# Performance work log

Hardware: AMD Instinct MI355X
Metric: run time of the kernel (lower is better)

Reference implementation:

```python
import jax, jax.numpy as jnp
import numpy as np


def setup_inputs() -> dict:
    key = jax.random.key(0)
    k1, k2, k3 = jax.random.split(key, 3)
    B, S_enc, S_dec, D = 8, 4096, 4096, 128
    b = jax.random.normal(k1, (B, S_enc, D), dtype=jnp.float32)
    h = jax.random.normal(k2, (B, S_dec, D), dtype=jnp.float32)
    W_b = jax.random.normal(k3, (D, D), dtype=jnp.float32) * (1.0 / np.sqrt(D))
    return {"b": b, "h": h, "W_b": W_b}


def reference(b, h, W_b):
    # tmp1 = h @ W_b : [B, S_dec, D]
    tmp1 = jnp.einsum('btd,de->bte', h, W_b)
    # scores = tmp1 @ b^T : [B, S_dec, S_enc]
    scores = jnp.einsum('bte,bse->bts', tmp1, b)
    attn = jax.nn.softmax(scores, axis=-1)
    # weighted sum over encoder positions (the original does this via a huge
    # tile/broadcast/multiply/reduce_sum; math is a batched matmul)
    cxt = jnp.einsum('bts,bsd->btd', attn, b)
    return cxt
```

## Files before the change

kernel.cpp:

```cpp
#include <hip/hip_runtime.h>

typedef _Float16 half2v __attribute__((ext_vector_type(2)));
typedef _Float16 half4 __attribute__((ext_vector_type(4)));
typedef _Float16 half8 __attribute__((ext_vector_type(8)));
typedef float floatx4 __attribute__((ext_vector_type(4)));

#define B_   8
#define SE   4096
#define SD   4096
#define D_   128
#define NT   64
#define LDB  136
#define LOG2E 1.44269504f

__device__ __forceinline__ void cp16_async(const _Float16* g, _Float16* l) {
    __builtin_amdgcn_global_load_lds((const __attribute__((address_space(1))) unsigned int*)g,
                                     (__attribute__((address_space(3))) unsigned int*)l, 16, 0, 0);
}

__global__ __launch_bounds__(256) void wprep(const float* __restrict__ W,
                                             _Float16* __restrict__ W16,
                                             _Float16* __restrict__ Wlo) {
    int i = blockIdx.x * 256 + threadIdx.x;
    float w = W[i];
    _Float16 hi = (_Float16)w;
    W16[i] = hi;
    Wlo[i] = (_Float16)(w - (float)hi);
}

__global__ __launch_bounds__(256) void kvprep(const float* __restrict__ b,
                                              const _Float16* __restrict__ W16,
                                              const _Float16* __restrict__ Wlo,
                                              _Float16* __restrict__ kp,
                                              _Float16* __restrict__ vT) {
    __shared__ _Float16 bs[64 * LDB];
    const int bb = blockIdx.y, s0 = blockIdx.x * 64;
    const int tid = threadIdx.x, wave = tid >> 6, lane = tid & 63;
    const int l15 = lane & 15, quad = lane >> 4;

    const float* bg = b + ((size_t)bb * SE + s0) * D_;
    #pragma unroll
    for (int it = 0; it < 4; ++it) {
        int idx = tid + it * 256;
        int row = idx >> 4, seg = idx & 15;
        const float* src = bg + row * D_ + seg * 8;
        float4 a = *(const float4*)src;
        float4 c = *(const float4*)(src + 4);
        half8 hv;
        hv[0] = (_Float16)a.x; hv[1] = (_Float16)a.y; hv[2] = (_Float16)a.z; hv[3] = (_Float16)a.w;
        hv[4] = (_Float16)c.x; hv[5] = (_Float16)c.y; hv[6] = (_Float16)c.z; hv[7] = (_Float16)c.w;
        *(half8*)(bs + row * LDB + seg * 8) = hv;
    }
    __syncthreads();

    half8 af[4];
    #pragma unroll
    for (int ks = 0; ks < 4; ++ks)
        af[ks] = *(const half8*)(bs + (wave * 16 + l15) * LDB + ks * 32 + quad * 8);
    floatx4 acc[8];
    #pragma unroll
    for (int nt = 0; nt < 8; ++nt) acc[nt] = (floatx4){0.f, 0.f, 0.f, 0.f};
    #pragma unroll
    for (int ks = 0; ks < 4; ++ks) {
        #pragma unroll
        for (int nt = 0; nt < 8; ++nt) {
            half8 bh = *(const half8*)(W16 + (size_t)(nt * 16 + l15) * 128 + ks * 32 + quad * 8);
            half8 bl = *(const half8*)(Wlo + (size_t)(nt * 16 + l15) * 128 + ks * 32 + quad * 8);
            acc[nt] = __builtin_amdgcn_mfma_f32_16x16x32_f16(af[ks], bh, acc[nt], 0, 0, 0);
            acc[nt] = __builtin_amdgcn_mfma_f32_16x16x32_f16(af[ks], bl, acc[nt], 0, 0, 0);
        }
    }

    {
        const int sq = tid & 15, dg = tid >> 4;
        half8 rowv[4];
        #pragma unroll
        for (int j = 0; j < 4; ++j)
            rowv[j] = *(const half8*)(bs + (sq * 4 + j) * LDB + dg * 8);
        #pragma unroll
        for (int r = 0; r < 8; ++r) {
            int d = dg * 8 + r;
            half4 o;
            #pragma unroll
            for (int j = 0; j < 4; ++j) o[j] = rowv[j][r];
            *(half4*)(vT + ((size_t)bb * D_ + d) * SE + s0 + sq * 4) = o;
        }
    }
    __syncthreads();

    #pragma unroll
    for (int nt = 0; nt < 8; ++nt)
        #pragma unroll
        for (int r = 0; r < 4; ++r)
            bs[(wave * 16 + quad * 4 + r) * LDB + nt * 16 + l15] = (_Float16)acc[nt][r];
    __syncthreads();
    _Float16* kg = kp + ((size_t)bb * SE + s0) * D_;
    {
        const int row = tid >> 2;
        #pragma unroll
        for (int it = 0; it < 4; ++it) {
            int ch = (tid & 3) + it * 4;
            half8 v = *(const half8*)(bs + row * LDB + ch * 8);
            *(half8*)(kg + row * D_ + ch * 8) = v;
        }
    }
}

__global__ __launch_bounds__(512, 4) void flash(const float* __restrict__ h,
                                                const _Float16* __restrict__ k,
                                                const _Float16* __restrict__ vT,
                                                float* __restrict__ out) {
    __shared__ _Float16 KV[2][16384];

    const int bb   = blockIdx.y;
    const int q0   = blockIdx.x * 64;
    const int tid  = threadIdx.x;
    const int wave = tid >> 6;
    const int wq   = wave >> 1;
    const int ws   = wave & 1;
    const int lane = tid & 63;
    const int l15  = lane & 15;
    const int quad = lane >> 4;

    const _Float16* kbase = k + (size_t)bb * SE * D_;
    const _Float16* vbase = vT + (size_t)bb * D_ * SE;

    int koff[2], voff[2];
    #pragma unroll
    for (int it = 0; it < 2; ++it) {
        int i = it * 512 + wave * 64 + lane;
        int kr = i >> 4, kpp = i & 15;
        koff[it] = kr * D_ + (kpp ^ (kr & 15)) * 8;
        int vr = i >> 3, vpp = i & 7;
        voff[it] = vr * SE + (vpp ^ (vr & 7)) * 8;
    }

    const _Float16* kA0[4]; const _Float16* kA1[4];
    const _Float16* vB0[2]; const _Float16* vB1[2];
    #pragma unroll
    for (int ks = 0; ks < 4; ++ks) {
        int o = l15 * 128 + (((ks * 4 + quad) ^ l15) * 8) + ws * 4096;
        kA0[ks] = &KV[0][o]; kA1[ks] = &KV[1][o];
    }
    #pragma unroll
    for (int stl = 0; stl < 2; ++stl) {
        int o = 8192 + l15 * 64 + (((ws * 4 + stl * 2 + (quad >> 1)) ^ (l15 & 7)) * 8) + (quad & 1) * 4;
        vB0[stl] = &KV[0][o]; vB1[stl] = &KV[1][o];
    }

    {
        _Float16* buf0 = &KV[0][0];
        #pragma unroll
        for (int it = 0; it < 2; ++it) {
            cp16_async(kbase + koff[it], buf0 + (it * 512 + wave * 64) * 8);
            cp16_async(vbase + voff[it], buf0 + 8192 + (it * 512 + wave * 64) * 8);
        }
    }

    half8 qf[4];
    {
        const float* hrow = h + ((size_t)bb * SD + q0 + wq * 16 + l15) * D_;
        #pragma unroll
        for (int ks = 0; ks < 4; ++ks) {
            float4 a = *(const float4*)(hrow + ks * 32 + quad * 8);
            float4 c = *(const float4*)(hrow + ks * 32 + quad * 8 + 4);
            half8 f;
            f[0] = (_Float16)(a.x * LOG2E); f[1] = (_Float16)(a.y * LOG2E);
            f[2] = (_Float16)(a.z * LOG2E); f[3] = (_Float16)(a.w * LOG2E);
            f[4] = (_Float16)(c.x * LOG2E); f[5] = (_Float16)(c.y * LOG2E);
            f[6] = (_Float16)(c.z * LOG2E); f[7] = (_Float16)(c.w * LOG2E);
            qf[ks] = f;
        }
    }

    floatx4 acc_o[8];
    #pragma unroll
    for (int dt = 0; dt < 8; ++dt) acc_o[dt] = (floatx4){0.f, 0.f, 0.f, 0.f};
    float m_q = -1e30f;
    float l_part = 0.f;
    const half2v one2 = { (_Float16)1.f, (_Float16)1.f };

    for (int t = 0; t < SE / NT; ++t) {
        __syncthreads();
        if (t + 1 < SE / NT) {
            const _Float16* kt = kbase + (size_t)(t + 1) * (NT * D_);
            const _Float16* vt = vbase + (size_t)(t + 1) * NT;
            _Float16* bufn = &KV[(t + 1) & 1][0];
            #pragma unroll
            for (int it = 0; it < 2; ++it) {
                cp16_async(kt + koff[it], bufn + (it * 512 + wave * 64) * 8);
                cp16_async(vt + voff[it], bufn + 8192 + (it * 512 + wave * 64) * 8);
            }
        }
        const bool odd = (t & 1) != 0;
        const _Float16* vB[2];
        vB[0] = odd ? vB1[0] : vB0[0];
        vB[1] = odd ? vB1[1] : vB0[1];

        floatx4 accs[2];
        accs[0] = (floatx4){0.f, 0.f, 0.f, 0.f};
        accs[1] = (floatx4){0.f, 0.f, 0.f, 0.f};
        #pragma unroll
        for (int ks = 0; ks < 4; ++ks) {
            const _Float16* ka = odd ? kA1[ks] : kA0[ks];
            half8 af0 = *(const half8*)(ka);
            half8 af1 = *(const half8*)(ka + 2048);
            accs[0] = __builtin_amdgcn_mfma_f32_16x16x32_f16(af0, qf[ks], accs[0], 0, 0, 0);
            accs[1] = __builtin_amdgcn_mfma_f32_16x16x32_f16(af1, qf[ks], accs[1], 0, 0, 0);
        }

        float mv = fmaxf(fmaxf(fmaxf(accs[0][0], accs[0][1]), fmaxf(accs[0][2], accs[0][3])),
                         fmaxf(fmaxf(accs[1][0], accs[1][1]), fmaxf(accs[1][2], accs[1][3])));
        if (__ballot(mv > m_q + 11.5f) != 0ull) {
            float m = mv;
            m = fmaxf(m, __shfl_xor(m, 16, 64));
            m = fmaxf(m, __shfl_xor(m, 32, 64));
            float mnew = fmaxf(m_q, m);
            float alpha = exp2f(m_q - mnew);
            l_part *= alpha;
            float ab[4];
            #pragma unroll
            for (int r = 0; r < 4; ++r) ab[r] = __shfl(alpha, quad * 4 + r, 64);
            #pragma unroll
            for (int dt = 0; dt < 8; ++dt)
                #pragma unroll
                for (int r = 0; r < 4; ++r) acc_o[dt][r] *= ab[r];
            m_q = mnew;
        }

        half4 pf[2];
        #pragma unroll
        for (int stl = 0; stl < 2; ++stl) {
            float p0 = exp2f(accs[stl][0] - m_q);
            float p1 = exp2f(accs[stl][1] - m_q);
            float p2 = exp2f(accs[stl][2] - m_q);
            float p3 = exp2f(accs[stl][3] - m_q);
            half2v lo = __builtin_bit_cast(half2v, __builtin_amdgcn_cvt_pkrtz(p0, p1));
            half2v hi = __builtin_bit_cast(half2v, __builtin_amdgcn_cvt_pkrtz(p2, p3));
#if __has_builtin(__builtin_amdgcn_fdot2)
            l_part = __builtin_amdgcn_fdot2(lo, one2, l_part, false);
            l_part = __builtin_amdgcn_fdot2(hi, one2, l_part, false);
#else
            l_part += p0 + p1 + p2 + p3;
#endif
            half4 pv; pv[0] = lo[0]; pv[1] = lo[1]; pv[2] = hi[0]; pv[3] = hi[1];
            pf[stl] = pv;
        }

        #pragma unroll
        for (int stl = 0; stl < 2; ++stl) {
            #pragma unroll
            for (int dt = 0; dt < 8; ++dt) {
                half4 vf = *(const half4*)(vB[stl] + dt * 1024);
                acc_o[dt] = __builtin_amdgcn_mfma_f32_16x16x16f16(pf[stl], vf, acc_o[dt], 0, 0, 0);
            }
        }
    }

    float l_own;
    {
        float l = l_part;
        l += __shfl_xor(l, 16, 64);
        l += __shfl_xor(l, 32, 64);
        l_own = l;
    }

    __syncthreads();
    float* Ob = (float*)&KV[0][0];
    float* ml = (float*)&KV[1][0];

    if (ws == 1) {
        #pragma unroll
        for (int dt = 0; dt < 8; ++dt)
            *(floatx4*)(Ob + ((wq * 8 + dt) * 64 + lane) * 4) = acc_o[dt];
        if (quad == 0)
            *(float2*)(ml + (wq * 16 + l15) * 2) = make_float2(m_q, l_own);
    }
    __syncthreads();
    if (ws == 0) {
        float m0r[4], l0r[4], m1r[4], l1r[4];
        #pragma unroll
        for (int r = 0; r < 4; ++r) {
            m0r[r] = __shfl(m_q, quad * 4 + r, 64);
            l0r[r] = __shfl(l_own, quad * 4 + r, 64);
            float2 p = *(float2*)(ml + (wq * 16 + quad * 4 + r) * 2);
            m1r[r] = p.x; l1r[r] = p.y;
        }
        float a0[4], a1[4], inv[4];
        #pragma unroll
        for (int r = 0; r < 4; ++r) {
            float mm = fmaxf(m0r[r], m1r[r]);
            a0[r] = exp2f(m0r[r] - mm);
            a1[r] = exp2f(m1r[r] - mm);
            inv[r] = 1.f / (l0r[r] * a0[r] + l1r[r] * a1[r]);
        }
        float* orow = out + ((size_t)bb * SD + q0 + wq * 16 + quad * 4) * D_;
        #pragma unroll
        for (int dt = 0; dt < 8; ++dt) {
            floatx4 o1 = *(floatx4*)(Ob + ((wq * 8 + dt) * 64 + lane) * 4);
            #pragma unroll
            for (int r = 0; r < 4; ++r)
                orow[(size_t)r * D_ + dt * 16 + l15] =
                    (acc_o[dt][r] * a0[r] + o1[r] * a1[r]) * inv[r];
        }
    }
}

extern "C" void kernel_launch(void* const* d_in, const int* in_sizes, int n_in,
                              void* d_out, int out_size, void* d_ws, size_t ws_size,
                              hipStream_t stream) {
    const float* b = (const float*)d_in[0];
    const float* h = (const float*)d_in[1];
    const float* W = (const float*)d_in[2];
    float* out = (float*)d_out;

    _Float16* W16 = (_Float16*)d_ws;
    _Float16* Wlo = W16 + 128 * 128;
    _Float16* kp  = Wlo + 128 * 128;
    _Float16* vT  = kp + (size_t)B_ * SE * D_;

    wprep<<<64, 256, 0, stream>>>(W, W16, Wlo);
    kvprep<<<dim3(SE / 64, B_), 256, 0, stream>>>(b, W16, Wlo, kp, vT);
    flash<<<dim3(SD / 64, B_), 512, 0, stream>>>(h, kp, vT, out);
}
```

Before: 204.4 us.

## Permute K rows to fuse PV into 16x16x32 MFMAs and fold max into accumulator init

Changes the K tile's global-to-LDS row mapping so the two 16-row score blocks line up as a single 32-wide P operand. The PV product then runs as 8 MFMA 16x16x32 ops per tile instead of 16 MFMA 16x16x16 ops. The running max is kept as a negated offset used to initialise the score accumulators, which removes the per-element subtraction before exp2. The loop is unrolled by two so the double-buffer pointers are chosen at compile time. The row permutation and V read layout must stay consistent, and any mismatch would corrupt results.

```diff
diff --git a/kernel.cpp b/kernel.cpp
--- a/kernel.cpp
+++ b/kernel.cpp
@@ -16,6 +16,14 @@
 __device__ __forceinline__ void cp16_async(const _Float16* g, _Float16* l) {
     __builtin_amdgcn_global_load_lds((const __attribute__((address_space(1))) unsigned int*)g,
                                      (__attribute__((address_space(3))) unsigned int*)l, 16, 0, 0);
+}
+
+__device__ __forceinline__ float dot2acc(half2v a, half2v b, float c) {
+#if __has_builtin(__builtin_amdgcn_fdot2)
+    return __builtin_amdgcn_fdot2(a, b, c, false);
+#else
+    return c + (float)a[0] * (float)b[0] + (float)a[1] * (float)b[1];
+#endif
 }
 
 __global__ __launch_bounds__(256) void wprep(const float* __restrict__ W,
@@ -130,22 +138,23 @@
     for (int it = 0; it < 2; ++it) {
         int i = it * 512 + wave * 64 + lane;
         int kr = i >> 4, kpp = i & 15;
-        koff[it] = kr * D_ + (kpp ^ (kr & 15)) * 8;
+        int km = kr & 15;
+        int srow = (kr & 32) + ((km >> 2) << 3) + (((kr >> 4) & 1) << 2) + (km & 3);
+        koff[it] = srow * D_ + ((kpp ^ km) * 8);
         int vr = i >> 3, vpp = i & 7;
-        voff[it] = vr * SE + (vpp ^ (vr & 7)) * 8;
+        voff[it] = vr * SE + ((vpp ^ (vr & 7)) * 8);
     }
 
     const _Float16* kA0[4]; const _Float16* kA1[4];
-    const _Float16* vB0[2]; const _Float16* vB1[2];
+    const _Float16 *vB0, *vB1;
     #pragma unroll
     for (int ks = 0; ks < 4; ++ks) {
         int o = l15 * 128 + (((ks * 4 + quad) ^ l15) * 8) + ws * 4096;
         kA0[ks] = &KV[0][o]; kA1[ks] = &KV[1][o];
     }
-    #pragma unroll
-    for (int stl = 0; stl < 2; ++stl) {
-        int o = 8192 + l15 * 64 + (((ws * 4 + stl * 2 + (quad >> 1)) ^ (l15 & 7)) * 8) + (quad & 1) * 4;
-        vB0[stl] = &KV[0][o]; vB1[stl] = &KV[1][o];
+    {
+        int o = 8192 + l15 * 64 + (((ws * 4 + quad) ^ (l15 & 7)) * 8);
+        vB0 = &KV[0][o]; vB1 = &KV[1][o];
     }
 
     {
@@ -176,87 +185,89 @@
     floatx4 acc_o[8];
     #pragma unroll
     for (int dt = 0; dt < 8; ++dt) acc_o[dt] = (floatx4){0.f, 0.f, 0.f, 0.f};
-    float m_q = -1e30f;
+    float nm = 0.f;
     float l_part = 0.f;
     const half2v one2 = { (_Float16)1.f, (_Float16)1.f };
 
-    for (int t = 0; t < SE / NT; ++t) {
-        __syncthreads();
-        if (t + 1 < SE / NT) {
-            const _Float16* kt = kbase + (size_t)(t + 1) * (NT * D_);
-            const _Float16* vt = vbase + (size_t)(t + 1) * NT;
-            _Float16* bufn = &KV[(t + 1) & 1][0];
-            #pragma unroll
-            for (int it = 0; it < 2; ++it) {
-                cp16_async(kt + koff[it], bufn + (it * 512 + wave * 64) * 8);
-                cp16_async(vt + voff[it], bufn + 8192 + (it * 512 + wave * 64) * 8);
-            }
-        }
-        const bool odd = (t & 1) != 0;
-        const _Float16* vB[2];
-        vB[0] = odd ? vB1[0] : vB0[0];
-        vB[1] = odd ? vB1[1] : vB0[1];
-
-        floatx4 accs[2];
-        accs[0] = (floatx4){0.f, 0.f, 0.f, 0.f};
-        accs[1] = (floatx4){0.f, 0.f, 0.f, 0.f};
-        #pragma unroll
-        for (int ks = 0; ks < 4; ++ks) {
-            const _Float16* ka = odd ? kA1[ks] : kA0[ks];
-            half8 af0 = *(const half8*)(ka);
-            half8 af1 = *(const half8*)(ka + 2048);
-            accs[0] = __builtin_amdgcn_mfma_f32_16x16x32_f16(af0, qf[ks], accs[0], 0, 0, 0);
-            accs[1] = __builtin_amdgcn_mfma_f32_16x16x32_f16(af1, qf[ks], accs[1], 0, 0, 0);
-        }
-
-        float mv = fmaxf(fmaxf(fmaxf(accs[0][0], accs[0][1]), fmaxf(accs[0][2], accs[0][3])),
-                         fmaxf(fmaxf(accs[1][0], accs[1][1]), fmaxf(accs[1][2], accs[1][3])));
-        if (__ballot(mv > m_q + 11.5f) != 0ull) {
-            float m = mv;
-            m = fmaxf(m, __shfl_xor(m, 16, 64));
-            m = fmaxf(m, __shfl_xor(m, 32, 64));
-            float mnew = fmaxf(m_q, m);
-            float alpha = exp2f(m_q - mnew);
-            l_part *= alpha;
-            float ab[4];
-            #pragma unroll
-            for (int r = 0; r < 4; ++r) ab[r] = __shfl(alpha, quad * 4 + r, 64);
-            #pragma unroll
-            for (int dt = 0; dt < 8; ++dt)
-                #pragma unroll
-                for (int r = 0; r < 4; ++r) acc_o[dt][r] *= ab[r];
-            m_q = mnew;
-        }
-
-        half4 pf[2];
-        #pragma unroll
-        for (int stl = 0; stl < 2; ++stl) {
-            float p0 = exp2f(accs[stl][0] - m_q);
-            float p1 = exp2f(accs[stl][1] - m_q);
-            float p2 = exp2f(accs[stl][2] - m_q);
-            float p3 = exp2f(accs[stl][3] - m_q);
-            half2v lo = __builtin_bit_cast(half2v, __builtin_amdgcn_cvt_pkrtz(p0, p1));
-            half2v hi = __builtin_bit_cast(half2v, __builtin_amdgcn_cvt_pkrtz(p2, p3));
-#if __has_builtin(__builtin_amdgcn_fdot2)
-            l_part = __builtin_amdgcn_fdot2(lo, one2, l_part, false);
-            l_part = __builtin_amdgcn_fdot2(hi, one2, l_part, false);
-#else
-            l_part += p0 + p1 + p2 + p3;
-#endif
-            half4 pv; pv[0] = lo[0]; pv[1] = lo[1]; pv[2] = hi[0]; pv[3] = hi[1];
-            pf[stl] = pv;
-        }
-
-        #pragma unroll
-        for (int stl = 0; stl < 2; ++stl) {
-            #pragma unroll
-            for (int dt = 0; dt < 8; ++dt) {
-                half4 vf = *(const half4*)(vB[stl] + dt * 1024);
-                acc_o[dt] = __builtin_amdgcn_mfma_f32_16x16x16f16(pf[stl], vf, acc_o[dt], 0, 0, 0);
-            }
-        }
-    }
-
+#define STEP(T, KA, VBP, NBUF)                                                        \
+  {                                                                                   \
+    __syncthreads();                  \
+    if ((T) + 1 < SE / NT) {                                                          \
+      const _Float16* kt = kbase + (size_t)((T) + 1) * (NT * D_);                     \
+      const _Float16* vt = vbase + (size_t)((T) + 1) * NT;                            \
+      _Float16* bufn = (NBUF);                                                        \
+      _Pragma("unroll")                                                               \
+      for (int it = 0; it < 2; ++it) {                                                \
+        cp16_async(kt + koff[it], bufn + (it * 512 + wave * 64) * 8);                 \
+        cp16_async(vt + voff[it], bufn + 8192 + (it * 512 + wave * 64) * 8);          \
+      }                                                                               \
+    }                                                                                 \
+                        \
+    floatx4 accs[2];                                                                  \
+    accs[0] = (floatx4){nm, nm, nm, nm};                                              \
+    accs[1] = accs[0];                                                                \
+    _Pragma("unroll")                                                                 \
+    for (int ks = 0; ks < 4; ++ks) {                                                  \
+      half8 af0 = *(const half8*)(KA[ks]);                                            \
+      half8 af1 = *(const half8*)(KA[ks] + 2048);                                     \
+      accs[0] = __builtin_amdgcn_mfma_f32_16x16x32_f16(af0, qf[ks], accs[0], 0, 0, 0);\
+      accs[1] = __builtin_amdgcn_mfma_f32_16x16x32_f16(af1, qf[ks], accs[1], 0, 0, 0);\
+    }                                                                                 \
+                                     \
+    float x0 = fmaxf(fmaxf(accs[0][0], accs[0][1]), accs[0][2]);                      \
+    float x1 = fmaxf(fmaxf(accs[0][3], accs[1][0]), accs[1][1]);                      \
+    float x2 = fmaxf(fmaxf(accs[1][2], accs[1][3]), x0);                              \
+    float mv = fmaxf(x1, x2);                                                         \
+    if (__ballot(mv > 11.5f) != 0ull) {              \
+      float mr = fmaxf(mv, __shfl_xor(mv, 16, 64));                                   \
+      mr = fmaxf(mr, __shfl_xor(mr, 32, 64));                                         \
+      float delta = fmaxf(mr, 0.f);                                                   \
+      float alpha = exp2f(-delta);                                                    \
+      l_part *= alpha;                                                                \
+      float ab[4];                                                                    \
+      _Pragma("unroll")                                                               \
+      for (int r = 0; r < 4; ++r) ab[r] = __shfl(alpha, quad * 4 + r, 64);            \
+      _Pragma("unroll")                                                               \
+      for (int dt = 0; dt < 8; ++dt)                                                  \
+        _Pragma("unroll")                                                             \
+        for (int r = 0; r < 4; ++r) acc_o[dt][r] *= ab[r];                            \
+      _Pragma("unroll")                                                               \
+      for (int stl = 0; stl < 2; ++stl)                                               \
+        _Pragma("unroll")                                                             \
+        for (int r = 0; r < 4; ++r) accs[stl][r] -= delta;                            \
+      nm -= delta;                                                                    \
+    }                                                                                 \
+         \
+    float p0 = exp2f(accs[0][0]), p1 = exp2f(accs[0][1]);                             \
+    float p2 = exp2f(accs[0][2]), p3 = exp2f(accs[0][3]);                             \
+    float p4 = exp2f(accs[1][0]), p5 = exp2f(accs[1][1]);                             \
+    float p6 = exp2f(accs[1][2]), p7 = exp2f(accs[1][3]);                             \
+    half2v c0 = __builtin_bit_cast(half2v, __builtin_amdgcn_cvt_pkrtz(p0, p1));       \
+    half2v c1 = __builtin_bit_cast(half2v, __builtin_amdgcn_cvt_pkrtz(p2, p3));       \
+    half2v c2 = __builtin_bit_cast(half2v, __builtin_amdgcn_cvt_pkrtz(p4, p5));       \
+    half2v c3 = __builtin_bit_cast(half2v, __builtin_amdgcn_cvt_pkrtz(p6, p7));       \
+    l_part = dot2acc(c0, one2, l_part);                                               \
+    l_part = dot2acc(c1, one2, l_part);                                               \
+    l_part = dot2acc(c2, one2, l_part);                                               \
+    l_part = dot2acc(c3, one2, l_part);                                               \
+    half8 pA;                                                                         \
+    pA[0] = c0[0]; pA[1] = c0[1]; pA[2] = c1[0]; pA[3] = c1[1];                       \
+    pA[4] = c2[0]; pA[5] = c2[1]; pA[6] = c3[0]; pA[7] = c3[1];                       \
+         \
+    _Pragma("unroll")                                                                 \
+    for (int dt = 0; dt < 8; ++dt) {                                                  \
+      half8 vf = *(const half8*)((VBP) + dt * 1024);                                  \
+      acc_o[dt] = __builtin_amdgcn_mfma_f32_16x16x32_f16(pA, vf, acc_o[dt], 0, 0, 0); \
+    }                                                                                 \
+  }
+
+    for (int t = 0; t < SE / NT; t += 2) {
+        STEP(t,     kA0, vB0, &KV[1][0]);
+        STEP(t + 1, kA1, vB1, &KV[0][0]);
+    }
+#undef STEP
+
+    const float m_q = -nm;
     float l_own;
     {
         float l = l_part;
```

Measured after the change: 191.0 us. -6.6%, faster.
